# Performance work log

Measured on AMD Instinct MI355X. Metric: run time of the kernel, lower is better.

## Reference

```python
import jax, jax.numpy as jnp
import numpy as np

HEAD_NUM = 16
SCALE = 1.0 / np.sqrt(HEAD_NUM)  # source divides by sqrt(head_num), not head_dim
MASK_VAL = -10000000.0


def setup_inputs() -> dict:
    key = jax.random.key(0)
    kq, kk, kv = jax.random.split(key, 3)
    shape = (2, 16, 2048, 64)  # [B, H, L, D]
    Q = jax.random.normal(kq, shape, dtype=jnp.float32)
    K = jax.random.normal(kk, shape, dtype=jnp.float32)
    V = jax.random.normal(kv, shape, dtype=jnp.float32)
    return {"Q": Q, "K": K, "V": V}


def reference(Q, K, V):
    L = Q.shape[-2]
    # [B, H, L, M] attention logits, scaled by 1/sqrt(head_num)
    logits = jnp.einsum('bhld,bhmd->bhlm', Q, K) * SCALE
    # causal mask: strictly-upper triangle gets -1e7 (additive, as in source)
    mask = jnp.triu(jnp.ones((L, L), dtype=logits.dtype), 1) * MASK_VAL
    logits = logits + mask[None, None, :, :]
    weights = jax.nn.softmax(logits, axis=-1)
    return jnp.einsum('bhlm,bhmd->bhld', weights, V)
```

## Files before the change

kernel.cpp:

```cpp
#include <hip/hip_runtime.h>
#include <hip/hip_bf16.h>

#define BM 128
#define BN 64
#define HD 64
#define LQ 2048
#define QSCALE 0.360673760222241f

typedef __attribute__((ext_vector_type(8))) short short8;
typedef __attribute__((ext_vector_type(4))) float f32x4;

static __device__ __forceinline__ unsigned pk2(float a, float b) {
    union { __hip_bfloat162 h2; unsigned u; } c;
    c.h2 = __float22bfloat162_rn(make_float2(a, b));
    return c.u;
}

__global__ __launch_bounds__(512, 2)
void fa_fwd(const float* __restrict__ Qg,
            const float* __restrict__ Kg,
            const float* __restrict__ Vg,
            float* __restrict__ Og) {
    __shared__ unsigned short sK[2][BN][64];
    __shared__ unsigned short sVt[2][HD][64];
    __shared__ unsigned short sP[8][16][64];

    const int t    = threadIdx.x;
    const int w    = t >> 6;
    const int lane = t & 63;
    const int qd   = lane >> 4;
    const int l    = lane & 15;
    const int l7   = l & 7;

    const int bx  = blockIdx.x;
    const int qt  = 15 - (bx >> 5);
    const int bh  = bx & 31;
    const int q0  = qt * BM;

    const size_t base = (size_t)bh * (LQ * HD);
    const float* Kp = Kg + base;
    const float* Vp = Vg + base;

    const int qrow = q0 + w * 16 + l;

    short8 bq[2];
    {
        const float* qp = Qg + base + (size_t)qrow * HD;
#pragma unroll
        for (int ks = 0; ks < 2; ++ks) {
            const float4 a = *(const float4*)(qp + ks * 32 + qd * 8);
            const float4 b = *(const float4*)(qp + ks * 32 + qd * 8 + 4);
            union { short8 s; uint4 u; } cv;
            cv.u.x = pk2(a.x * QSCALE, a.y * QSCALE);
            cv.u.y = pk2(a.z * QSCALE, a.w * QSCALE);
            cv.u.z = pk2(b.x * QSCALE, b.y * QSCALE);
            cv.u.w = pk2(b.z * QSCALE, b.w * QSCALE);
            bq[ks] = cv.s;
        }
    }

    const int r0   = t >> 4;
    const int c4   = (t & 15) * 4;
    const int ko   = c4 >> 3;
    const int koff = c4 & 7;
    const int RA   = w * 4;

    float4 kf[2], vf[2];
    auto issue = [&](int kv0) {
        kf[0] = *(const float4*)(Kp + (size_t)(kv0 + r0) * HD + c4);
        kf[1] = *(const float4*)(Kp + (size_t)(kv0 + 32 + r0) * HD + c4);
        vf[0] = *(const float4*)(Vp + (size_t)(kv0 + RA + qd) * HD + c4);
        vf[1] = *(const float4*)(Vp + (size_t)(kv0 + 32 + RA + qd) * HD + c4);
    };

    auto commit = [&](int buf) {
#pragma unroll
        for (int p = 0; p < 2; ++p) {
            const int r = p * 32 + r0;
            uint2 u; u.x = pk2(kf[p].x, kf[p].y); u.y = pk2(kf[p].z, kf[p].w);
            *(uint2*)&sK[buf][r][((ko ^ (r & 7)) << 3) + koff] = u;
        }
#pragma unroll
        for (int p = 0; p < 2; ++p) {
            float e0 = vf[p].x, e1 = vf[p].y, e2 = vf[p].z, e3 = vf[p].w;
            float s0 = (qd & 2) ? e0 : e2;
            float s1 = (qd & 2) ? e1 : e3;
            s0 = __shfl_xor(s0, 32); s1 = __shfl_xor(s1, 32);
            if (qd & 2) { e0 = s0; e1 = s1; } else { e2 = s0; e3 = s1; }
            s0 = (qd & 1) ? e0 : e1;
            s1 = (qd & 1) ? e2 : e3;
            s0 = __shfl_xor(s0, 16); s1 = __shfl_xor(s1, 16);
            if (qd & 1) { e0 = s0; e2 = s1; } else { e1 = s0; e3 = s1; }
            const int d = c4 + qd;
            const int R = p * 32 + RA;
            uint2 u; u.x = pk2(e0, e1); u.y = pk2(e2, e3);
            *(uint2*)&sVt[buf][d][(((R >> 3) ^ (d & 7)) << 3) + (R & 4)] = u;
        }
    };

    f32x4 accO[4];
#pragma unroll
    for (int mt = 0; mt < 4; ++mt) accO[mt] = (f32x4){0.f, 0.f, 0.f, 0.f};
    float lsum = 0.f;

    const int qminw = q0 + w * 16;
    const int qmaxw = qminw + 15;
    const int n_it  = (q0 + BM) / BN;

    issue(0);
    commit(0);

    for (int it = 0; it < n_it; ++it) {
        const int kv0 = it * BN;
        const int buf = it & 1;
        __syncthreads();
        const bool more = (it + 1 < n_it);
        if (more) issue(kv0 + BN);

        if (kv0 <= qmaxw) {
            f32x4 accS[4];
#pragma unroll
            for (int mt = 0; mt < 4; ++mt) accS[mt] = (f32x4){0.f, 0.f, 0.f, 0.f};
#pragma unroll
            for (int ks = 0; ks < 2; ++ks) {
#pragma unroll
                for (int mt = 0; mt < 4; ++mt) {
                    const int row = mt * 16 + l;
                    const short8 ak = *(const short8*)
                        &sK[buf][row][(((ks * 4 + qd) ^ l7)) << 3];
                    accS[mt] = __builtin_amdgcn_mfma_f32_16x16x32_bf16(ak, bq[ks], accS[mt], 0, 0, 0);
                }
            }

            if (kv0 + BN - 1 > qminw) {
#pragma unroll
                for (int mt = 0; mt < 4; ++mt) {
                    const int kvr = kv0 + mt * 16 + qd * 4;
#pragma unroll
                    for (int r = 0; r < 4; ++r)
                        if (kvr + r > qrow) accS[mt][r] = -1e30f;
                }
            }

#pragma unroll
            for (int mt = 0; mt < 4; ++mt) {
                const float p0 = __builtin_amdgcn_exp2f(accS[mt][0]);
                const float p1 = __builtin_amdgcn_exp2f(accS[mt][1]);
                const float p2 = __builtin_amdgcn_exp2f(accS[mt][2]);
                const float p3 = __builtin_amdgcn_exp2f(accS[mt][3]);
                lsum += (p0 + p1) + (p2 + p3);
                uint2 u; u.x = pk2(p0, p1); u.y = pk2(p2, p3);
                const int oct = 2 * mt + (qd >> 1);
                *(uint2*)&sP[w][l][((oct ^ l7) << 3) + ((qd & 1) << 2)] = u;
            }
            asm volatile("s_waitcnt lgkmcnt(0)" ::: "memory");

#pragma unroll
            for (int ks = 0; ks < 2; ++ks) {
                const short8 bp = *(const short8*)
                    &sP[w][l][(((ks * 4 + qd) ^ l7)) << 3];
#pragma unroll
                for (int mt = 0; mt < 4; ++mt) {
                    const int row = mt * 16 + l;
                    const short8 av = *(const short8*)
                        &sVt[buf][row][(((ks * 4 + qd) ^ l7)) << 3];
                    accO[mt] = __builtin_amdgcn_mfma_f32_16x16x32_bf16(av, bp, accO[mt], 0, 0, 0);
                }
            }
        }

        if (more) commit(buf ^ 1);
    }

    lsum += __shfl_xor(lsum, 16);
    lsum += __shfl_xor(lsum, 32);
    const float inv = 1.0f / lsum;
    float* Op = Og + base + (size_t)qrow * HD;
#pragma unroll
    for (int mt = 0; mt < 4; ++mt) {
        float4 o;
        o.x = accO[mt][0] * inv; o.y = accO[mt][1] * inv;
        o.z = accO[mt][2] * inv; o.w = accO[mt][3] * inv;
        *(float4*)(Op + mt * 16 + qd * 4) = o;
    }
}

extern "C" void kernel_launch(void* const* d_in, const int* in_sizes, int n_in,
                              void* d_out, int out_size, void* d_ws, size_t ws_size,
                              hipStream_t stream) {
    const float* Q = (const float*)d_in[0];
    const float* K = (const float*)d_in[1];
    const float* V = (const float*)d_in[2];
    float* O = (float*)d_out;
    fa_fwd<<<dim3(512), dim3(512), 0, stream>>>(Q, K, V, O);
}
```

Measured before the change: 131.1 us.

## Double KV tile to 128 rows, reorder block scheduling, move barrier after prefetch

Raises the KV tile from 64 to 128 rows, so each iteration loads and commits twice as much K/V and handles it in two 64-row halves with a wider XOR swizzle on the transposed V buffer. This halves the number of barriers and loop iterations per block. It also interleaves block-to-q-tile assignment so the second half of the grid runs short q-tiles first, and it issues the next global prefetch before the barrier. In exchange, LDS use and register pressure for the prefetch buffers go up, which may lower occupancy.

```diff
diff --git a/kernel.cpp b/kernel.cpp
--- a/kernel.cpp
+++ b/kernel.cpp
@@ -2,7 +2,7 @@
 #include <hip/hip_bf16.h>
 
 #define BM 128
-#define BN 64
+#define BN 128
 #define HD 64
 #define LQ 2048
 #define QSCALE 0.360673760222241f
@@ -22,7 +22,7 @@
             const float* __restrict__ Vg,
             float* __restrict__ Og) {
     __shared__ unsigned short sK[2][BN][64];
-    __shared__ unsigned short sVt[2][HD][64];
+    __shared__ unsigned short sVt[2][HD][BN];
     __shared__ unsigned short sP[8][16][64];
 
     const int t    = threadIdx.x;
@@ -33,7 +33,8 @@
     const int l7   = l & 7;
 
     const int bx  = blockIdx.x;
-    const int qt  = 15 - (bx >> 5);
+    const int idx = (bx >> 5) & 7;
+    const int qt  = (bx & 256) ? idx : (15 - idx);
     const int bh  = bx & 31;
     const int q0  = qt * BM;
 
@@ -65,23 +66,25 @@
     const int koff = c4 & 7;
     const int RA   = w * 4;
 
-    float4 kf[2], vf[2];
+    float4 kf[4], vf[4];
     auto issue = [&](int kv0) {
-        kf[0] = *(const float4*)(Kp + (size_t)(kv0 + r0) * HD + c4);
-        kf[1] = *(const float4*)(Kp + (size_t)(kv0 + 32 + r0) * HD + c4);
-        vf[0] = *(const float4*)(Vp + (size_t)(kv0 + RA + qd) * HD + c4);
-        vf[1] = *(const float4*)(Vp + (size_t)(kv0 + 32 + RA + qd) * HD + c4);
+#pragma unroll
+        for (int p = 0; p < 4; ++p)
+            kf[p] = *(const float4*)(Kp + (size_t)(kv0 + p * 32 + r0) * HD + c4);
+#pragma unroll
+        for (int p = 0; p < 4; ++p)
+            vf[p] = *(const float4*)(Vp + (size_t)(kv0 + p * 32 + RA + qd) * HD + c4);
     };
 
     auto commit = [&](int buf) {
 #pragma unroll
-        for (int p = 0; p < 2; ++p) {
+        for (int p = 0; p < 4; ++p) {
             const int r = p * 32 + r0;
             uint2 u; u.x = pk2(kf[p].x, kf[p].y); u.y = pk2(kf[p].z, kf[p].w);
             *(uint2*)&sK[buf][r][((ko ^ (r & 7)) << 3) + koff] = u;
         }
 #pragma unroll
-        for (int p = 0; p < 2; ++p) {
+        for (int p = 0; p < 4; ++p) {
             float e0 = vf[p].x, e1 = vf[p].y, e2 = vf[p].z, e3 = vf[p].w;
             float s0 = (qd & 2) ? e0 : e2;
             float s1 = (qd & 2) ? e1 : e3;
@@ -94,7 +97,7 @@
             const int d = c4 + qd;
             const int R = p * 32 + RA;
             uint2 u; u.x = pk2(e0, e1); u.y = pk2(e2, e3);
-            *(uint2*)&sVt[buf][d][(((R >> 3) ^ (d & 7)) << 3) + (R & 4)] = u;
+            *(uint2*)&sVt[buf][d][(((R >> 3) ^ (d & 15)) << 3) + (R & 4)] = u;
         }
     };
 
@@ -105,7 +108,7 @@
 
     const int qminw = q0 + w * 16;
     const int qmaxw = qminw + 15;
-    const int n_it  = (q0 + BM) / BN;
+    const int n_it  = qt + 1;
 
     issue(0);
     commit(0);
@@ -113,11 +116,15 @@
     for (int it = 0; it < n_it; ++it) {
         const int kv0 = it * BN;
         const int buf = it & 1;
-        __syncthreads();
         const bool more = (it + 1 < n_it);
         if (more) issue(kv0 + BN);
-
-        if (kv0 <= qmaxw) {
+        __syncthreads();
+
+#pragma unroll
+        for (int h2 = 0; h2 < 2; ++h2) {
+            const int kvh0 = kv0 + h2 * 64;
+            if (kvh0 > qmaxw) continue;
+
             f32x4 accS[4];
 #pragma unroll
             for (int mt = 0; mt < 4; ++mt) accS[mt] = (f32x4){0.f, 0.f, 0.f, 0.f};
@@ -125,17 +132,17 @@
             for (int ks = 0; ks < 2; ++ks) {
 #pragma unroll
                 for (int mt = 0; mt < 4; ++mt) {
-                    const int row = mt * 16 + l;
+                    const int row = h2 * 64 + mt * 16 + l;
                     const short8 ak = *(const short8*)
-                        &sK[buf][row][(((ks * 4 + qd) ^ l7)) << 3];
+                        &sK[buf][row][((ks * 4 + qd) ^ l7) << 3];
                     accS[mt] = __builtin_amdgcn_mfma_f32_16x16x32_bf16(ak, bq[ks], accS[mt], 0, 0, 0);
                 }
             }
 
-            if (kv0 + BN - 1 > qminw) {
+            if (kvh0 + 63 > qminw) {
 #pragma unroll
                 for (int mt = 0; mt < 4; ++mt) {
-                    const int kvr = kv0 + mt * 16 + qd * 4;
+                    const int kvr = kvh0 + mt * 16 + qd * 4;
 #pragma unroll
                     for (int r = 0; r < 4; ++r)
                         if (kvr + r > qrow) accS[mt][r] = -1e30f;
@@ -158,12 +165,13 @@
 #pragma unroll
             for (int ks = 0; ks < 2; ++ks) {
                 const short8 bp = *(const short8*)
-                    &sP[w][l][(((ks * 4 + qd) ^ l7)) << 3];
+                    &sP[w][l][((ks * 4 + qd) ^ l7) << 3];
 #pragma unroll
                 for (int mt = 0; mt < 4; ++mt) {
-                    const int row = mt * 16 + l;
+                    const int vrow = mt * 16 + l;
+                    const int o    = h2 * 8 + ks * 4 + qd;
                     const short8 av = *(const short8*)
-                        &sVt[buf][row][(((ks * 4 + qd) ^ l7)) << 3];
+                        &sVt[buf][vrow][(o ^ l) << 3];
                     accO[mt] = __builtin_amdgcn_mfma_f32_16x16x32_bf16(av, bp, accO[mt], 0, 0, 0);
                 }
             }
```

Result: slower. 142.1 us (+8.4%).
